# Optimization experiments

Measured on AMD Instinct MI355X. Metric: run time of the kernel, lower is better.

The kernel has to match this reference:

```python
import jax, jax.numpy as jnp
import numpy as np

B, H, D, MAX_N = 2048, 1024, 512, 64
MID_DEC, MID_SP, MID_CD = 768, 512, 512  # build_mlp midmult=1.0 -> mid=(in+out)/2


def setup_inputs() -> dict:
    key = jax.random.key(0)
    ks = jax.random.split(key, 8)
    s = 0.02
    return {
        "z": jax.random.normal(ks[0], (B, H), jnp.float32),
        "key_table": jax.random.normal(ks[1], (MAX_N, H), jnp.float32),
        "sp_w1": jax.random.normal(ks[2], (H, MID_SP), jnp.float32) * s,
        "sp_b1": jnp.zeros((MID_SP,), jnp.float32),
        "sp_g": jnp.ones((MID_SP,), jnp.float32),
        "sp_beta": jnp.zeros((MID_SP,), jnp.float32),
        "sp_w2": jax.random.normal(ks[3], (MID_SP, 1), jnp.float32) * s,
        "sp_b2": jnp.ones((1,), jnp.float32) * 32.0,  # bias so predicted n is mid-range
        "cd_w1": jax.random.normal(ks[4], (1, MID_CD), jnp.float32) * s,
        "cd_b1": jnp.zeros((MID_CD,), jnp.float32),
        "cd_w2": jax.random.normal(ks[5], (MID_CD, H), jnp.float32) * s,
        "cd_b2": jnp.zeros((H,), jnp.float32),
        "dec_w1": jax.random.normal(ks[6], (H, MID_DEC), jnp.float32) * s,
        "dec_b1": jnp.zeros((MID_DEC,), jnp.float32),
        "dec_w2": jax.random.normal(ks[7], (MID_DEC, D), jnp.float32) * s,
        "dec_b2": jnp.zeros((D,), jnp.float32),
    }


def mish(x):
    return x * jnp.tanh(jax.nn.softplus(x))


def layernorm(x, g, b, eps=1e-5):
    mu = x.mean(-1, keepdims=True)
    var = x.var(-1, keepdims=True)
    return (x - mu) * jax.lax.rsqrt(var + eps) * g + b


def reference(z, key_table, sp_w1, sp_b1, sp_g, sp_beta, sp_w2, sp_b2,
              cd_w1, cd_b1, cd_w2, cd_b2, dec_w1, dec_b1, dec_w2, dec_b2):
    # size_pred MLP: Linear -> LayerNorm -> Mish -> Linear
    h = mish(layernorm(z @ sp_w1 + sp_b1, sp_g, sp_beta))
    n_logits = h @ sp_w2 + sp_b2                                  # [B, 1]
    n = jnp.clip(jnp.round(n_logits[:, 0]).astype(jnp.int32), 0, MAX_N)
    n = jax.lax.stop_gradient(n)                                  # int in torch -> no grad
    # shared.cardinality(n): scalar count -> hidden encoding
    nf = n[:, None].astype(z.dtype)
    n_enc = mish(nf @ cd_w1 + cd_b1) @ cd_w2 + cd_b2              # [B, H]
    zc = z - n_enc
    # ragged repeat_interleave + get_key, padded to MAX_N with a validity mask
    kidx = jnp.arange(MAX_N)                                      # positions 0..MAX_N-1
    mask = kidx[None, :] < n[:, None]                             # [B, MAX_N]
    zp = zc[:, None, :] * key_table[None, :, :]                   # [B, MAX_N, H]
    # decoder MLP: Linear -> Mish -> Linear
    x = mish(zp @ dec_w1 + dec_b1) @ dec_w2 + dec_b2              # [B, MAX_N, D]
    x = jnp.where(mask[..., None], x, 0.0).reshape(B * MAX_N, D)
    batch = jnp.where(mask, jnp.arange(B)[:, None], -1).reshape(B * MAX_N)
    return x, batch
```

## Files before the change

kernel.cpp:

```cpp
#include <hip/hip_runtime.h>
#include <stdint.h>

typedef unsigned short ushort_t;
typedef unsigned int uint_t;

#define H_SZ   1024
#define D_OUT  512
#define MAXN   64
#define MIDSP  512
#define MIDCD  512
#define MIDDEC 768

typedef __bf16 bf16x8 __attribute__((ext_vector_type(8)));
typedef float  f32x4  __attribute__((ext_vector_type(4)));

static __device__ __forceinline__ float asf(uint_t u) { union { uint_t i; float f; } c; c.i = u; return c.f; }
static __device__ __forceinline__ uint_t rnbf(float f) {
  union { uint_t i; float f; } c; c.f = f;
  return (c.i + 0x7fffu + ((c.i >> 16) & 1u)) >> 16;
}
static __device__ __forceinline__ ushort_t f2bf(float f) { return (ushort_t)rnbf(f); }
static __device__ __forceinline__ float bf2f(float f) { return asf(rnbf(f) << 16); }
static __device__ __forceinline__ uint_t mul2bf(uint_t a, uint_t b) {
  float a0 = asf(a << 16), a1 = asf(a & 0xffff0000u);
  float b0 = asf(b << 16), b1 = asf(b & 0xffff0000u);
  return rnbf(a0 * b0) | (rnbf(a1 * b1) << 16);
}
static __device__ __forceinline__ double mish_d(double x) { return x * tanh(log1p(exp(x))); }
static __device__ __forceinline__ float mish_f(float x) {
  float t = __expf(x);
  float u = t * t + 2.f * t;
  float r = u / (u + 2.f);
  return (x > 30.f) ? x : x * r;
}

__global__ __launch_bounds__(256) void k_pack1(const float* __restrict__ w1,
                                               ushort_t* __restrict__ pk1) {
  const int t8 = blockIdx.x * 256 + threadIdx.x;
  const int lane = t8 & 63;
  const int ks = (t8 >> 6) & 31;
  const int wp = t8 >> 11;
  const int w = wp / 6, p = wp % 6;
  const int q = lane >> 4, l15 = lane & 15;
  const int row = p * 128 + w * 16 + l15;
  const int colb = ks * 32 + q * 8;
  ushort_t v[8];
#pragma unroll
  for (int e = 0; e < 8; ++e) v[e] = f2bf(w1[(size_t)(colb + e) * 768 + row]);
  *(uint4*)(pk1 + (size_t)t8 * 8) = *(const uint4*)v;
}

__global__ __launch_bounds__(256) void k_pack2(const float* __restrict__ w2,
                                               ushort_t* __restrict__ pk2) {
  const int t8 = blockIdx.x * 256 + threadIdx.x;
  const int lane = t8 & 63;
  const int ki = (t8 >> 6) & 15;
  const int wp = t8 >> 10;
  const int w = wp / 6, p = wp % 6;
  const int ksl = ki >> 2, i = ki & 3;
  const int q = lane >> 4, l15 = lane & 15;
  const int row = w * 64 + i * 16 + l15;
  const int colb = p * 128 + ksl * 32 + q * 8;
  ushort_t v[8];
#pragma unroll
  for (int e = 0; e < 8; ++e) v[e] = f2bf(w2[(size_t)(colb + e) * 512 + row]);
  *(uint4*)(pk2 + (size_t)t8 * 8) = *(const uint4*)v;
}

__global__ __launch_bounds__(256) void k_cvtkey(const float* __restrict__ src, ushort_t* __restrict__ dst) {
  const int i = blockIdx.x * 1024 + threadIdx.x;
#pragma unroll
  for (int j = 0; j < 4; ++j) dst[i + j * 256] = f2bf(src[i + j * 256]);
}

__global__ __launch_bounds__(256) void k_enc(const float* __restrict__ w1, const float* __restrict__ b1,
                                             const float* __restrict__ w2, const float* __restrict__ b2,
                                             float* __restrict__ enc) {
  const int v = blockIdx.x, t = threadIdx.x;
  const int c = blockIdx.y * 256 + t;
  __shared__ float m[MIDCD];
  for (int i = t; i < MIDCD; i += 256) {
    double a = (double)v * (double)w1[i] + (double)b1[i];
    m[i] = (float)mish_d(a);
  }
  __syncthreads();
  double s = (double)b2[c];
  for (int k = 0; k < MIDCD; ++k) s += (double)m[k] * (double)w2[(size_t)k * H_SZ + c];
  enc[(size_t)v * H_SZ + c] = (float)s;
}

__global__ __launch_bounds__(256) void k_npath(
    const float* __restrict__ z, const float* __restrict__ w1, const float* __restrict__ b1,
    const float* __restrict__ g, const float* __restrict__ be,
    const float* __restrict__ w2, const float* __restrict__ b2,
    const float* __restrict__ enc, int* __restrict__ nbuf,
    ushort_t* __restrict__ zc, float* __restrict__ outb) {
  const int t = threadIdx.x;
  const int r0 = blockIdx.x * 4;
  const int lane = t & 63, wv = t >> 6;
  __shared__ float zs[4][H_SZ];
  __shared__ double wred[4];
  __shared__ int n4[4];

#pragma unroll
  for (int i = 0; i < 16; ++i) {
    const int idx = i * 256 + t;
    zs[idx >> 10][idx & 1023] = z[(size_t)r0 * H_SZ + idx];
  }
  __syncthreads();

  const int c0 = t, c1 = t + 256;
  float a0[4], a1[4];
#pragma unroll
  for (int r = 0; r < 4; ++r) { a0[r] = 0.f; a1[r] = 0.f; }

  for (int k = 0; k < H_SZ; k += 4) {
    float4 zr[4];
#pragma unroll
    for (int r = 0; r < 4; ++r) zr[r] = *(const float4*)&zs[r][k];
#pragma unroll
    for (int kk = 0; kk < 4; ++kk) {
      const float w0 = w1[(size_t)(k + kk) * MIDSP + c0];
      const float w1v = w1[(size_t)(k + kk) * MIDSP + c1];
#pragma unroll
      for (int r = 0; r < 4; ++r) {
        const float zk = ((const float*)&zr[r])[kk];
        a0[r] += zk * w0;
        a1[r] += zk * w1v;
      }
    }
  }

  auto block_sum = [&](double v) -> double {
#pragma unroll
    for (int off = 32; off > 0; off >>= 1) v += __shfl_down(v, off, 64);
    if (lane == 0) wred[wv] = v;
    __syncthreads();
    const double s = wred[0] + wred[1] + wred[2] + wred[3];
    __syncthreads();
    return s;
  };

  const double bia0 = (double)b1[c0], bia1 = (double)b1[c1];
  const double g0 = (double)g[c0], g1 = (double)g[c1];
  const double be0 = (double)be[c0], be1 = (double)be[c1];
  const double wv0 = (double)w2[c0], wv1 = (double)w2[c1];
  const double b2v = (double)b2[0];

  for (int r = 0; r < 4; ++r) {
    const double x0 = (double)a0[r] + bia0;
    const double x1 = (double)a1[r] + bia1;
    const double mu = block_sum(x0 + x1) * (1.0 / 512.0);
    const double varr = block_sum((x0 - mu) * (x0 - mu) + (x1 - mu) * (x1 - mu)) * (1.0 / 512.0);
    const double rs = 1.0 / sqrt(varr + 1e-5);
    const double h0 = mish_d((x0 - mu) * rs * g0 + be0);
    const double h1 = mish_d((x1 - mu) * rs * g1 + be1);
    const double logit = block_sum(h0 * wv0 + h1 * wv1) + b2v;
    if (t == 0) n4[r] = (int)fmin(64.0, fmax(0.0, rint(logit)));
  }
  __syncthreads();

  if (t < 4) nbuf[r0 + t] = n4[t];
  {
    const int r = t >> 6, j = t & 63;
    outb[(size_t)(r0 + r) * MAXN + j] = (j < n4[r]) ? (float)(r0 + r) : -1.0f;
  }
#pragma unroll
  for (int i = 0; i < 16; ++i) {
    const int idx = i * 256 + t;
    const int r = idx >> 10, c = idx & 1023;
    zc[(size_t)(r0 + r) * H_SZ + c] = f2bf(zs[r][c] - enc[(size_t)n4[r] * H_SZ + c]);
  }
}

static __device__ __forceinline__ void dec_sweep2(
    char* sA, char* sT,
    const ushort_t* __restrict__ pk1, const float* __restrict__ db1,
    const ushort_t* __restrict__ pk2, const float* __restrict__ db2,
    float* __restrict__ ob, const int tid, const int lim) {
  const int lane = tid & 63;
  const int w = tid >> 6;
  const int q = lane >> 4;
  const int l15 = lane & 15;
  const int x7 = l15 & 7;

  f32x4 z4 = {0.f, 0.f, 0.f, 0.f};
  f32x4 acc2[2][4];
#pragma unroll
  for (int mt = 0; mt < 2; ++mt)
#pragma unroll
    for (int i = 0; i < 4; ++i) acc2[mt][i] = z4;

  for (int p = 0; p < 6; ++p) {
    f32x4 acc0 = z4, acc1 = z4;
    const ushort_t* bp1 = pk1 + ((size_t)(w * 6 + p) << 14) + lane * 8;
    const char* sa0 = sA + (size_t)l15 * 2048;

#pragma unroll 4
    for (int ks = 0; ks < 32; ++ks) {
      bf16x8 bfr = *(const bf16x8*)(bp1 + ks * 512);
      bf16x8 a0 = *(const bf16x8*)(sa0 + (((ks * 4 + q) ^ x7) * 16));
      bf16x8 a1 = *(const bf16x8*)(sa0 + 16 * 2048 + (((ks * 4 + q) ^ x7) * 16));
      acc0 = __builtin_amdgcn_mfma_f32_16x16x32_bf16(a0, bfr, acc0, 0, 0, 0);
      acc1 = __builtin_amdgcn_mfma_f32_16x16x32_bf16(a1, bfr, acc1, 0, 0, 0);
    }

    {
      const int pl = w * 16 + l15;
      const float bias = db1[p * 128 + pl];
      const int c = pl >> 3;
      const int off = (pl & 7) * 2;
#pragma unroll
      for (int r = 0; r < 4; ++r) {
        const int j0 = q * 4 + r;
        *(ushort_t*)(sT + j0 * 256 + ((c ^ (j0 & 7)) * 16 + off)) = f2bf(mish_f(acc0[r] + bias));
        const int j1 = 16 + q * 4 + r;
        *(ushort_t*)(sT + j1 * 256 + ((c ^ (j1 & 7)) * 16 + off)) = f2bf(mish_f(acc1[r] + bias));
      }
    }
    __syncthreads();

    const ushort_t* bp2 = pk2 + ((size_t)(w * 6 + p) << 13) + lane * 8;
    const char* st0 = sT + (size_t)l15 * 256;
#pragma unroll
    for (int ksl = 0; ksl < 4; ++ksl) {
      bf16x8 bfr[4];
#pragma unroll
      for (int i = 0; i < 4; ++i) bfr[i] = *(const bf16x8*)(bp2 + (ksl * 4 + i) * 512);
      bf16x8 a0 = *(const bf16x8*)(st0 + (((ksl * 4 + q) ^ x7) * 16));
      bf16x8 a1 = *(const bf16x8*)(st0 + 16 * 256 + (((ksl * 4 + q) ^ x7) * 16));
#pragma unroll
      for (int i = 0; i < 4; ++i) {
        acc2[0][i] = __builtin_amdgcn_mfma_f32_16x16x32_bf16(a0, bfr[i], acc2[0][i], 0, 0, 0);
        acc2[1][i] = __builtin_amdgcn_mfma_f32_16x16x32_bf16(a1, bfr[i], acc2[1][i], 0, 0, 0);
      }
    }
    __syncthreads();
  }

#pragma unroll
  for (int mt = 0; mt < 2; ++mt)
#pragma unroll
    for (int i = 0; i < 4; ++i) {
      const int col = (w * 4 + i) * 16 + l15;
      const float bias = db2[col];
#pragma unroll
      for (int r = 0; r < 4; ++r) {
        const int j = mt * 16 + q * 4 + r;
        const float v = (j < lim) ? bf2f(acc2[mt][i][r] + bias) : 0.f;
        ob[(size_t)j * D_OUT + col] = v;
      }
    }
}

__global__ __launch_bounds__(512, 4) void k_dec(
    const ushort_t* __restrict__ key, const ushort_t* __restrict__ pk1,
    const float* __restrict__ db1, const ushort_t* __restrict__ pk2,
    const float* __restrict__ db2, const ushort_t* __restrict__ zc,
    const int* __restrict__ nbuf, float* __restrict__ out) {
  __shared__ char sA[65536];
  __shared__ char sT[8192];

  const int tid = threadIdx.x;
  const int b = blockIdx.x;

  int n = nbuf[b];
  n = n < 0 ? 0 : (n > MAXN ? MAXN : n);
  float* ob = out + (size_t)b * (MAXN * D_OUT);

  if (n == 0) {
    const float4 z4f = make_float4(0.f, 0.f, 0.f, 0.f);
#pragma unroll
    for (int i = 0; i < 16; ++i) *(float4*)(ob + i * 2048 + tid * 4) = z4f;
    return;
  }

  const int gj = tid >> 4;
  const int gk = tid & 15;
  const ushort_t* zrow = zc + (size_t)b * H_SZ + gk * 8;
  char* awbase = sA + gj * 2048;
  const int xj = gj & 7;

  {
    const ushort_t* keyrow = key + (size_t)gj * H_SZ + gk * 8;
#pragma unroll
    for (int i = 0; i < 8; ++i) {
      const int c = i * 16 + gk;
      uint4 kv = *(const uint4*)(keyrow + i * 128);
      uint4 zv = *(const uint4*)(zrow + i * 128);
      uint4 r;
      r.x = mul2bf(kv.x, zv.x); r.y = mul2bf(kv.y, zv.y);
      r.z = mul2bf(kv.z, zv.z); r.w = mul2bf(kv.w, zv.w);
      *(uint4*)(awbase + ((c ^ xj) * 16)) = r;
    }
  }
  __syncthreads();
  {
    const int lim = n > 32 ? 32 : n;
    dec_sweep2(sA, sT, pk1, db1, pk2, db2, ob, tid, lim);
  }

  if (n > 32) {
    __syncthreads();
    const ushort_t* keyrow = key + (size_t)(32 + gj) * H_SZ + gk * 8;
#pragma unroll
    for (int i = 0; i < 8; ++i) {
      const int c = i * 16 + gk;
      uint4 kv = *(const uint4*)(keyrow + i * 128);
      uint4 zv = *(const uint4*)(zrow + i * 128);
      uint4 r;
      r.x = mul2bf(kv.x, zv.x); r.y = mul2bf(kv.y, zv.y);
      r.z = mul2bf(kv.z, zv.z); r.w = mul2bf(kv.w, zv.w);
      *(uint4*)(awbase + ((c ^ xj) * 16)) = r;
    }
    __syncthreads();
    dec_sweep2(sA, sT, pk1, db1, pk2, db2, ob + (size_t)32 * D_OUT, tid, n - 32);
  } else {
    float* oz = ob + 32 * D_OUT;
    const float4 z4f = make_float4(0.f, 0.f, 0.f, 0.f);
#pragma unroll
    for (int i = 0; i < 8; ++i) *(float4*)(oz + i * 2048 + tid * 4) = z4f;
  }
}

extern "C" void kernel_launch(void* const* d_in, const int* in_sizes, int n_in,
                              void* d_out, int out_size, void* d_ws, size_t ws_size,
                              hipStream_t stream) {
  const float* z      = (const float*)d_in[0];
  const float* key    = (const float*)d_in[1];
  const float* sp_w1  = (const float*)d_in[2];
  const float* sp_b1  = (const float*)d_in[3];
  const float* sp_g   = (const float*)d_in[4];
  const float* sp_be  = (const float*)d_in[5];
  const float* sp_w2  = (const float*)d_in[6];
  const float* sp_b2  = (const float*)d_in[7];
  const float* cd_w1  = (const float*)d_in[8];
  const float* cd_b1  = (const float*)d_in[9];
  const float* cd_w2  = (const float*)d_in[10];
  const float* cd_b2  = (const float*)d_in[11];
  const float* dec_w1 = (const float*)d_in[12];
  const float* dec_b1 = (const float*)d_in[13];
  const float* dec_w2 = (const float*)d_in[14];
  const float* dec_b2 = (const float*)d_in[15];

  char* ws = (char*)d_ws;
  float*    enc   = (float*)(ws + 0);
  int*      nbuf  = (int*)(ws + 266240);
  ushort_t* zc    = (ushort_t*)(ws + 274432);
  ushort_t* pk1   = (ushort_t*)(ws + 4468736);
  ushort_t* pk2   = (ushort_t*)(ws + 6041600);
  ushort_t* keyb  = (ushort_t*)(ws + 6828032);

  float* out  = (float*)d_out;
  float* outb = out + (size_t)2048 * MAXN * D_OUT;

  (void)in_sizes; (void)n_in; (void)out_size; (void)ws_size;

  k_pack1<<<384, 256, 0, stream>>>(dec_w1, pk1);
  k_pack2<<<192, 256, 0, stream>>>(dec_w2, pk2);
  k_cvtkey<<<64, 256, 0, stream>>>(key, keyb);
  k_enc<<<dim3(65, 4), 256, 0, stream>>>(cd_w1, cd_b1, cd_w2, cd_b2, enc);
  k_npath<<<512, 256, 0, stream>>>(z, sp_w1, sp_b1, sp_g, sp_be, sp_w2, sp_b2, enc, nbuf, zc, outb);
  k_dec<<<2048, 512, 0, stream>>>(keyb, pk1, dec_b1, pk2, dec_b2, zc, nbuf, out);
}
```

Measured before the change: 731.6 us.

## Decode two batch rows per block to reuse weight fragments; fuse prep kernels

The decoder kernel now handles two batch rows per workgroup, so each loaded weight fragment from both decoder layers feeds four MFMAs instead of two. This halves the weight traffic from L2/global per unit of work. In exchange, LDS use per block roughly doubles (about 144 KB), which allows fewer resident blocks per CU. The second 32-row phase also runs whenever either row of the pair needs it, and the n==0 early exit is gone. Separately, the three weight and key conversion kernels are merged into one launch to save launch overhead.

After: 778.5 us. 1.06x slower.

```diff
diff --git a/kernel.cpp b/kernel.cpp
--- a/kernel.cpp
+++ b/kernel.cpp
@@ -34,43 +34,42 @@
   return (x > 30.f) ? x : x * r;
 }
 
-__global__ __launch_bounds__(256) void k_pack1(const float* __restrict__ w1,
-                                               ushort_t* __restrict__ pk1) {
-  const int t8 = blockIdx.x * 256 + threadIdx.x;
-  const int lane = t8 & 63;
-  const int ks = (t8 >> 6) & 31;
-  const int wp = t8 >> 11;
-  const int w = wp / 6, p = wp % 6;
-  const int q = lane >> 4, l15 = lane & 15;
-  const int row = p * 128 + w * 16 + l15;
-  const int colb = ks * 32 + q * 8;
-  ushort_t v[8];
-#pragma unroll
-  for (int e = 0; e < 8; ++e) v[e] = f2bf(w1[(size_t)(colb + e) * 768 + row]);
-  *(uint4*)(pk1 + (size_t)t8 * 8) = *(const uint4*)v;
-}
-
-__global__ __launch_bounds__(256) void k_pack2(const float* __restrict__ w2,
-                                               ushort_t* __restrict__ pk2) {
-  const int t8 = blockIdx.x * 256 + threadIdx.x;
-  const int lane = t8 & 63;
-  const int ki = (t8 >> 6) & 15;
-  const int wp = t8 >> 10;
-  const int w = wp / 6, p = wp % 6;
-  const int ksl = ki >> 2, i = ki & 3;
-  const int q = lane >> 4, l15 = lane & 15;
-  const int row = w * 64 + i * 16 + l15;
-  const int colb = p * 128 + ksl * 32 + q * 8;
-  ushort_t v[8];
-#pragma unroll
-  for (int e = 0; e < 8; ++e) v[e] = f2bf(w2[(size_t)(colb + e) * 512 + row]);
-  *(uint4*)(pk2 + (size_t)t8 * 8) = *(const uint4*)v;
-}
-
-__global__ __launch_bounds__(256) void k_cvtkey(const float* __restrict__ src, ushort_t* __restrict__ dst) {
-  const int i = blockIdx.x * 1024 + threadIdx.x;
-#pragma unroll
-  for (int j = 0; j < 4; ++j) dst[i + j * 256] = f2bf(src[i + j * 256]);
+__global__ __launch_bounds__(256) void k_prep(const float* __restrict__ w1, ushort_t* __restrict__ pk1,
+                                              const float* __restrict__ w2, ushort_t* __restrict__ pk2,
+                                              const float* __restrict__ keysrc, ushort_t* __restrict__ keyb) {
+  const int bid = blockIdx.x;
+  if (bid < 384) {
+    const int t8 = bid * 256 + threadIdx.x;
+    const int lane = t8 & 63;
+    const int ks = (t8 >> 6) & 31;
+    const int wp = t8 >> 11;
+    const int w = wp / 6, p = wp % 6;
+    const int q = lane >> 4, l15 = lane & 15;
+    const int row = p * 128 + w * 16 + l15;
+    const int colb = ks * 32 + q * 8;
+    ushort_t v[8];
+#pragma unroll
+    for (int e = 0; e < 8; ++e) v[e] = f2bf(w1[(size_t)(colb + e) * 768 + row]);
+    *(uint4*)(pk1 + (size_t)t8 * 8) = *(const uint4*)v;
+  } else if (bid < 576) {
+    const int t8 = (bid - 384) * 256 + threadIdx.x;
+    const int lane = t8 & 63;
+    const int ki = (t8 >> 6) & 15;
+    const int wp = t8 >> 10;
+    const int w = wp / 6, p = wp % 6;
+    const int ksl = ki >> 2, i = ki & 3;
+    const int q = lane >> 4, l15 = lane & 15;
+    const int row = w * 64 + i * 16 + l15;
+    const int colb = p * 128 + ksl * 32 + q * 8;
+    ushort_t v[8];
+#pragma unroll
+    for (int e = 0; e < 8; ++e) v[e] = f2bf(w2[(size_t)(colb + e) * 512 + row]);
+    *(uint4*)(pk2 + (size_t)t8 * 8) = *(const uint4*)v;
+  } else {
+    const int i = (bid - 576) * 1024 + threadIdx.x;
+#pragma unroll
+    for (int j = 0; j < 4; ++j) keyb[i + j * 256] = f2bf(keysrc[i + j * 256]);
+  }
 }
 
 __global__ __launch_bounds__(256) void k_enc(const float* __restrict__ w1, const float* __restrict__ b1,
@@ -173,11 +172,12 @@
   }
 }
 
-static __device__ __forceinline__ void dec_sweep2(
+static __device__ __forceinline__ void dec_pair(
     char* sA, char* sT,
     const ushort_t* __restrict__ pk1, const float* __restrict__ db1,
     const ushort_t* __restrict__ pk2, const float* __restrict__ db2,
-    float* __restrict__ ob, const int tid, const int lim) {
+    float* __restrict__ ob0, float* __restrict__ ob1,
+    const int tid, const int lim0, const int lim1) {
   const int lane = tid & 63;
   const int w = tid >> 6;
   const int q = lane >> 4;
@@ -185,24 +185,37 @@
   const int x7 = l15 & 7;
 
   f32x4 z4 = {0.f, 0.f, 0.f, 0.f};
-  f32x4 acc2[2][4];
-#pragma unroll
-  for (int mt = 0; mt < 2; ++mt)
-#pragma unroll
-    for (int i = 0; i < 4; ++i) acc2[mt][i] = z4;
+  f32x4 acc2[2][2][4];
+#pragma unroll
+  for (int bb = 0; bb < 2; ++bb)
+#pragma unroll
+    for (int mt = 0; mt < 2; ++mt)
+#pragma unroll
+      for (int i = 0; i < 4; ++i) acc2[bb][mt][i] = z4;
 
   for (int p = 0; p < 6; ++p) {
-    f32x4 acc0 = z4, acc1 = z4;
+    f32x4 acc[2][2];
+#pragma unroll
+    for (int bb = 0; bb < 2; ++bb)
+#pragma unroll
+      for (int mt = 0; mt < 2; ++mt) acc[bb][mt] = z4;
+
     const ushort_t* bp1 = pk1 + ((size_t)(w * 6 + p) << 14) + lane * 8;
-    const char* sa0 = sA + (size_t)l15 * 2048;
+    const char* saA = sA + (size_t)l15 * 2048;
+    const char* saB = sA + 65536 + (size_t)l15 * 2048;
 
 #pragma unroll 4
     for (int ks = 0; ks < 32; ++ks) {
       bf16x8 bfr = *(const bf16x8*)(bp1 + ks * 512);
-      bf16x8 a0 = *(const bf16x8*)(sa0 + (((ks * 4 + q) ^ x7) * 16));
-      bf16x8 a1 = *(const bf16x8*)(sa0 + 16 * 2048 + (((ks * 4 + q) ^ x7) * 16));
-      acc0 = __builtin_amdgcn_mfma_f32_16x16x32_bf16(a0, bfr, acc0, 0, 0, 0);
-      acc1 = __builtin_amdgcn_mfma_f32_16x16x32_bf16(a1, bfr, acc1, 0, 0, 0);
+      const int co = ((ks * 4 + q) ^ x7) * 16;
+      bf16x8 a00 = *(const bf16x8*)(saA + co);
+      bf16x8 a01 = *(const bf16x8*)(saA + 16 * 2048 + co);
+      bf16x8 a10 = *(const bf16x8*)(saB + co);
+      bf16x8 a11 = *(const bf16x8*)(saB + 16 * 2048 + co);
+      acc[0][0] = __builtin_amdgcn_mfma_f32_16x16x32_bf16(a00, bfr, acc[0][0], 0, 0, 0);
+      acc[0][1] = __builtin_amdgcn_mfma_f32_16x16x32_bf16(a01, bfr, acc[0][1], 0, 0, 0);
+      acc[1][0] = __builtin_amdgcn_mfma_f32_16x16x32_bf16(a10, bfr, acc[1][0], 0, 0, 0);
+      acc[1][1] = __builtin_amdgcn_mfma_f32_16x16x32_bf16(a11, bfr, acc[1][1], 0, 0, 0);
     }
 
     {
@@ -211,115 +224,119 @@
       const int c = pl >> 3;
       const int off = (pl & 7) * 2;
 #pragma unroll
-      for (int r = 0; r < 4; ++r) {
-        const int j0 = q * 4 + r;
-        *(ushort_t*)(sT + j0 * 256 + ((c ^ (j0 & 7)) * 16 + off)) = f2bf(mish_f(acc0[r] + bias));
-        const int j1 = 16 + q * 4 + r;
-        *(ushort_t*)(sT + j1 * 256 + ((c ^ (j1 & 7)) * 16 + off)) = f2bf(mish_f(acc1[r] + bias));
-      }
+      for (int bb = 0; bb < 2; ++bb)
+#pragma unroll
+        for (int mt = 0; mt < 2; ++mt)
+#pragma unroll
+          for (int r = 0; r < 4; ++r) {
+            const int j = mt * 16 + q * 4 + r;
+            *(ushort_t*)(sT + bb * 8192 + j * 256 + ((c ^ (j & 7)) * 16 + off)) =
+                f2bf(mish_f(acc[bb][mt][r] + bias));
+          }
     }
     __syncthreads();
 
     const ushort_t* bp2 = pk2 + ((size_t)(w * 6 + p) << 13) + lane * 8;
-    const char* st0 = sT + (size_t)l15 * 256;
 #pragma unroll
     for (int ksl = 0; ksl < 4; ++ksl) {
       bf16x8 bfr[4];
 #pragma unroll
       for (int i = 0; i < 4; ++i) bfr[i] = *(const bf16x8*)(bp2 + (ksl * 4 + i) * 512);
-      bf16x8 a0 = *(const bf16x8*)(st0 + (((ksl * 4 + q) ^ x7) * 16));
-      bf16x8 a1 = *(const bf16x8*)(st0 + 16 * 256 + (((ksl * 4 + q) ^ x7) * 16));
+      const int co = ((ksl * 4 + q) ^ x7) * 16;
+      bf16x8 a00 = *(const bf16x8*)(sT + (size_t)l15 * 256 + co);
+      bf16x8 a01 = *(const bf16x8*)(sT + (size_t)(16 + l15) * 256 + co);
+      bf16x8 a10 = *(const bf16x8*)(sT + 8192 + (size_t)l15 * 256 + co);
+      bf16x8 a11 = *(const bf16x8*)(sT + 8192 + (size_t)(16 + l15) * 256 + co);
 #pragma unroll
       for (int i = 0; i < 4; ++i) {
-        acc2[0][i] = __builtin_amdgcn_mfma_f32_16x16x32_bf16(a0, bfr[i], acc2[0][i], 0, 0, 0);
-        acc2[1][i] = __builtin_amdgcn_mfma_f32_16x16x32_bf16(a1, bfr[i], acc2[1][i], 0, 0, 0);
+        acc2[0][0][i] = __builtin_amdgcn_mfma_f32_16x16x32_bf16(a00, bfr[i], acc2[0][0][i], 0, 0, 0);
+        acc2[0][1][i] = __builtin_amdgcn_mfma_f32_16x16x32_bf16(a01, bfr[i], acc2[0][1][i], 0, 0, 0);
+        acc2[1][0][i] = __builtin_amdgcn_mfma_f32_16x16x32_bf16(a10, bfr[i], acc2[1][0][i], 0, 0, 0);
+        acc2[1][1][i] = __builtin_amdgcn_mfma_f32_16x16x32_bf16(a11, bfr[i], acc2[1][1][i], 0, 0, 0);
       }
     }
     __syncthreads();
   }
 
 #pragma unroll
-  for (int mt = 0; mt < 2; ++mt)
-#pragma unroll
-    for (int i = 0; i < 4; ++i) {
-      const int col = (w * 4 + i) * 16 + l15;
-      const float bias = db2[col];
-#pragma unroll
-      for (int r = 0; r < 4; ++r) {
-        const int j = mt * 16 + q * 4 + r;
-        const float v = (j < lim) ? bf2f(acc2[mt][i][r] + bias) : 0.f;
-        ob[(size_t)j * D_OUT + col] = v;
+  for (int bb = 0; bb < 2; ++bb) {
+    float* ob = bb ? ob1 : ob0;
+    const int lim = bb ? lim1 : lim0;
+#pragma unroll
+    for (int mt = 0; mt < 2; ++mt)
+#pragma unroll
+      for (int i = 0; i < 4; ++i) {
+        const int col = (w * 4 + i) * 16 + l15;
+        const float bias = db2[col];
+#pragma unroll
+        for (int r = 0; r < 4; ++r) {
+          const int j = mt * 16 + q * 4 + r;
+          const float v = (j < lim) ? bf2f(acc2[bb][mt][i][r] + bias) : 0.f;
+          ob[(size_t)j * D_OUT + col] = v;
+        }
       }
-    }
-}
-
-__global__ __launch_bounds__(512, 4) void k_dec(
+  }
+}
+
+__global__ __launch_bounds__(512, 2) void k_dec(
     const ushort_t* __restrict__ key, const ushort_t* __restrict__ pk1,
     const float* __restrict__ db1, const ushort_t* __restrict__ pk2,
     const float* __restrict__ db2, const ushort_t* __restrict__ zc,
     const int* __restrict__ nbuf, float* __restrict__ out) {
-  __shared__ char sA[65536];
-  __shared__ char sT[8192];
+  __shared__ char sA[131072];
+  __shared__ char sT[16384];
 
   const int tid = threadIdx.x;
-  const int b = blockIdx.x;
-
-  int n = nbuf[b];
-  n = n < 0 ? 0 : (n > MAXN ? MAXN : n);
-  float* ob = out + (size_t)b * (MAXN * D_OUT);
-
-  if (n == 0) {
-    const float4 z4f = make_float4(0.f, 0.f, 0.f, 0.f);
-#pragma unroll
-    for (int i = 0; i < 16; ++i) *(float4*)(ob + i * 2048 + tid * 4) = z4f;
-    return;
-  }
-
-  const int gj = tid >> 4;
-  const int gk = tid & 15;
-  const ushort_t* zrow = zc + (size_t)b * H_SZ + gk * 8;
+  const int b0 = blockIdx.x * 2, b1 = b0 + 1;
+
+  int n0 = nbuf[b0]; n0 = n0 < 0 ? 0 : (n0 > MAXN ? MAXN : n0);
+  int n1 = nbuf[b1]; n1 = n1 < 0 ? 0 : (n1 > MAXN ? MAXN : n1);
+  float* ob0 = out + (size_t)b0 * (MAXN * D_OUT);
+  float* ob1 = out + (size_t)b1 * (MAXN * D_OUT);
+
+  const int gj = tid >> 3;
+  const int gk = tid & 7;
+  const int brow = gj & 31;
+  const ushort_t* zrow = zc + (size_t)(gj < 32 ? b0 : b1) * H_SZ + gk * 8;
   char* awbase = sA + gj * 2048;
   const int xj = gj & 7;
 
-  {
-    const ushort_t* keyrow = key + (size_t)gj * H_SZ + gk * 8;
-#pragma unroll
-    for (int i = 0; i < 8; ++i) {
-      const int c = i * 16 + gk;
-      uint4 kv = *(const uint4*)(keyrow + i * 128);
-      uint4 zv = *(const uint4*)(zrow + i * 128);
+  auto agen = [&](int ph) {
+    const ushort_t* keyrow = key + (size_t)(ph * 32 + brow) * H_SZ + gk * 8;
+#pragma unroll
+    for (int i = 0; i < 16; ++i) {
+      const int c = i * 8 + gk;
+      uint4 kv = *(const uint4*)(keyrow + i * 64);
+      uint4 zv = *(const uint4*)(zrow + i * 64);
       uint4 r;
       r.x = mul2bf(kv.x, zv.x); r.y = mul2bf(kv.y, zv.y);
       r.z = mul2bf(kv.z, zv.z); r.w = mul2bf(kv.w, zv.w);
       *(uint4*)(awbase + ((c ^ xj) * 16)) = r;
     }
-  }
+  };
+
+  agen(0);
   __syncthreads();
   {
-    const int lim = n > 32 ? 32 : n;
-    dec_sweep2(sA, sT, pk1, db1, pk2, db2, ob, tid, lim);
-  }
-
-  if (n > 32) {
-    __syncthreads();
-    const ushort_t* keyrow = key + (size_t)(32 + gj) * H_SZ + gk * 8;
+    const int l0 = n0 > 32 ? 32 : n0;
+    const int l1 = n1 > 32 ? 32 : n1;
+    dec_pair(sA, sT, pk1, db1, pk2, db2, ob0, ob1, tid, l0, l1);
+  }
+
+  if (n0 > 32 || n1 > 32) {
+    agen(1);
+    __syncthreads();
+    const int l0 = n0 > 32 ? n0 - 32 : 0;
+    const int l1 = n1 > 32 ? n1 - 32 : 0;
+    dec_pair(sA, sT, pk1, db1, pk2, db2,
+             ob0 + (size_t)32 * D_OUT, ob1 + (size_t)32 * D_OUT, tid, l0, l1);
+  } else {
+    const float4 z4f = make_float4(0.f, 0.f, 0.f, 0.f);
 #pragma unroll
     for (int i = 0; i < 8; ++i) {
-      const int c = i * 16 + gk;
-      uint4 kv = *(const uint4*)(keyrow + i * 128);
-      uint4 zv = *(const uint4*)(zrow + i * 128);
-      uint4 r;
-      r.x = mul2bf(kv.x, zv.x); r.y = mul2bf(kv.y, zv.y);
-      r.z = mul2bf(kv.z, zv.z); r.w = mul2bf(kv.w, zv.w);
-      *(uint4*)(awbase + ((c ^ xj) * 16)) = r;
-    }
-    __syncthreads();
-    dec_sweep2(sA, sT, pk1, db1, pk2, db2, ob + (size_t)32 * D_OUT, tid, n - 32);
-  } else {
-    float* oz = ob + 32 * D_OUT;
-    const float4 z4f = make_float4(0.f, 0.f, 0.f, 0.f);
-#pragma unroll
-    for (int i = 0; i < 8; ++i) *(float4*)(oz + i * 2048 + tid * 4) = z4f;
+      *(float4*)(ob0 + 32 * D_OUT + i * 2048 + tid * 4) = z4f;
+      *(float4*)(ob1 + 32 * D_OUT + i * 2048 + tid * 4) = z4f;
+    }
   }
 }
 
@@ -356,10 +373,8 @@
 
   (void)in_sizes; (void)n_in; (void)out_size; (void)ws_size;
 
-  k_pack1<<<384, 256, 0, stream>>>(dec_w1, pk1);
-  k_pack2<<<192, 256, 0, stream>>>(dec_w2, pk2);
-  k_cvtkey<<<64, 256, 0, stream>>>(key, keyb);
+  k_prep<<<640, 256, 0, stream>>>(dec_w1, pk1, dec_w2, pk2, key, keyb);
   k_enc<<<dim3(65, 4), 256, 0, stream>>>(cd_w1, cd_b1, cd_w2, cd_b2, enc);
   k_npath<<<512, 256, 0, stream>>>(z, sp_w1, sp_b1, sp_g, sp_be, sp_w2, sp_b2, enc, nbuf, zc, outb);
-  k_dec<<<2048, 512, 0, stream>>>(keyb, pk1, dec_b1, pk2, dec_b2, zc, nbuf, out);
-}
+  k_dec<<<1024, 512, 0, stream>>>(keyb, pk1, dec_b1, pk2, dec_b2, zc, nbuf, out);
+}
```

## Merge weight-prep kernels and compute three decoder N-panels per A-fragment load

Applied to the files above, without the earlier changes.

The three small prep kernels (w1 pack, w2 pack, key conversion) are merged into one launch selected by block index, removing two launch gaps. In the decoder sweep, the first GEMM now processes three 128-column panels at once, so each A fragment read from LDS feeds six MFMAs instead of two. The second GEMM still runs per panel. This cuts LDS reads and loop overhead in the first GEMM but adds accumulator and B-fragment registers under launch_bounds(512,4), which may cause spills or lower occupancy.

After: 789.0 us. 1.08x slower.

```diff
diff --git a/kernel.cpp b/kernel.cpp
--- a/kernel.cpp
+++ b/kernel.cpp
@@ -34,43 +34,42 @@
   return (x > 30.f) ? x : x * r;
 }
 
-__global__ __launch_bounds__(256) void k_pack1(const float* __restrict__ w1,
-                                               ushort_t* __restrict__ pk1) {
-  const int t8 = blockIdx.x * 256 + threadIdx.x;
-  const int lane = t8 & 63;
-  const int ks = (t8 >> 6) & 31;
-  const int wp = t8 >> 11;
-  const int w = wp / 6, p = wp % 6;
-  const int q = lane >> 4, l15 = lane & 15;
-  const int row = p * 128 + w * 16 + l15;
-  const int colb = ks * 32 + q * 8;
-  ushort_t v[8];
-#pragma unroll
-  for (int e = 0; e < 8; ++e) v[e] = f2bf(w1[(size_t)(colb + e) * 768 + row]);
-  *(uint4*)(pk1 + (size_t)t8 * 8) = *(const uint4*)v;
-}
-
-__global__ __launch_bounds__(256) void k_pack2(const float* __restrict__ w2,
-                                               ushort_t* __restrict__ pk2) {
-  const int t8 = blockIdx.x * 256 + threadIdx.x;
-  const int lane = t8 & 63;
-  const int ki = (t8 >> 6) & 15;
-  const int wp = t8 >> 10;
-  const int w = wp / 6, p = wp % 6;
-  const int ksl = ki >> 2, i = ki & 3;
-  const int q = lane >> 4, l15 = lane & 15;
-  const int row = w * 64 + i * 16 + l15;
-  const int colb = p * 128 + ksl * 32 + q * 8;
-  ushort_t v[8];
-#pragma unroll
-  for (int e = 0; e < 8; ++e) v[e] = f2bf(w2[(size_t)(colb + e) * 512 + row]);
-  *(uint4*)(pk2 + (size_t)t8 * 8) = *(const uint4*)v;
-}
-
-__global__ __launch_bounds__(256) void k_cvtkey(const float* __restrict__ src, ushort_t* __restrict__ dst) {
-  const int i = blockIdx.x * 1024 + threadIdx.x;
-#pragma unroll
-  for (int j = 0; j < 4; ++j) dst[i + j * 256] = f2bf(src[i + j * 256]);
+__global__ __launch_bounds__(256) void k_prep(const float* __restrict__ w1, ushort_t* __restrict__ pk1,
+                                              const float* __restrict__ w2, ushort_t* __restrict__ pk2,
+                                              const float* __restrict__ keysrc, ushort_t* __restrict__ keyb) {
+  const int bid = blockIdx.x;
+  if (bid < 384) {
+    const int t8 = bid * 256 + threadIdx.x;
+    const int lane = t8 & 63;
+    const int ks = (t8 >> 6) & 31;
+    const int wp = t8 >> 11;
+    const int w = wp / 6, p = wp % 6;
+    const int q = lane >> 4, l15 = lane & 15;
+    const int row = p * 128 + w * 16 + l15;
+    const int colb = ks * 32 + q * 8;
+    ushort_t v[8];
+#pragma unroll
+    for (int e = 0; e < 8; ++e) v[e] = f2bf(w1[(size_t)(colb + e) * 768 + row]);
+    *(uint4*)(pk1 + (size_t)t8 * 8) = *(const uint4*)v;
+  } else if (bid < 576) {
+    const int t8 = (bid - 384) * 256 + threadIdx.x;
+    const int lane = t8 & 63;
+    const int ki = (t8 >> 6) & 15;
+    const int wp = t8 >> 10;
+    const int w = wp / 6, p = wp % 6;
+    const int ksl = ki >> 2, i = ki & 3;
+    const int q = lane >> 4, l15 = lane & 15;
+    const int row = w * 64 + i * 16 + l15;
+    const int colb = p * 128 + ksl * 32 + q * 8;
+    ushort_t v[8];
+#pragma unroll
+    for (int e = 0; e < 8; ++e) v[e] = f2bf(w2[(size_t)(colb + e) * 512 + row]);
+    *(uint4*)(pk2 + (size_t)t8 * 8) = *(const uint4*)v;
+  } else {
+    const int i = (bid - 576) * 1024 + threadIdx.x;
+#pragma unroll
+    for (int j = 0; j < 4; ++j) keyb[i + j * 256] = f2bf(keysrc[i + j * 256]);
+  }
 }
 
 __global__ __launch_bounds__(256) void k_enc(const float* __restrict__ w1, const float* __restrict__ b1,
@@ -191,51 +190,70 @@
 #pragma unroll
     for (int i = 0; i < 4; ++i) acc2[mt][i] = z4;
 
-  for (int p = 0; p < 6; ++p) {
-    f32x4 acc0 = z4, acc1 = z4;
-    const ushort_t* bp1 = pk1 + ((size_t)(w * 6 + p) << 14) + lane * 8;
+  for (int g = 0; g < 2; ++g) {
+    f32x4 acc[3][2];
+#pragma unroll
+    for (int j = 0; j < 3; ++j)
+#pragma unroll
+      for (int mt = 0; mt < 2; ++mt) acc[j][mt] = z4;
+
+    const ushort_t* bpa = pk1 + ((size_t)(w * 6 + g * 3 + 0) << 14) + lane * 8;
+    const ushort_t* bpb = pk1 + ((size_t)(w * 6 + g * 3 + 1) << 14) + lane * 8;
+    const ushort_t* bpc = pk1 + ((size_t)(w * 6 + g * 3 + 2) << 14) + lane * 8;
     const char* sa0 = sA + (size_t)l15 * 2048;
 
 #pragma unroll 4
     for (int ks = 0; ks < 32; ++ks) {
-      bf16x8 bfr = *(const bf16x8*)(bp1 + ks * 512);
-      bf16x8 a0 = *(const bf16x8*)(sa0 + (((ks * 4 + q) ^ x7) * 16));
-      bf16x8 a1 = *(const bf16x8*)(sa0 + 16 * 2048 + (((ks * 4 + q) ^ x7) * 16));
-      acc0 = __builtin_amdgcn_mfma_f32_16x16x32_bf16(a0, bfr, acc0, 0, 0, 0);
-      acc1 = __builtin_amdgcn_mfma_f32_16x16x32_bf16(a1, bfr, acc1, 0, 0, 0);
-    }
-
-    {
-      const int pl = w * 16 + l15;
-      const float bias = db1[p * 128 + pl];
-      const int c = pl >> 3;
-      const int off = (pl & 7) * 2;
-#pragma unroll
-      for (int r = 0; r < 4; ++r) {
-        const int j0 = q * 4 + r;
-        *(ushort_t*)(sT + j0 * 256 + ((c ^ (j0 & 7)) * 16 + off)) = f2bf(mish_f(acc0[r] + bias));
-        const int j1 = 16 + q * 4 + r;
-        *(ushort_t*)(sT + j1 * 256 + ((c ^ (j1 & 7)) * 16 + off)) = f2bf(mish_f(acc1[r] + bias));
+      const int co = ((ks * 4 + q) ^ x7) * 16;
+      bf16x8 a0 = *(const bf16x8*)(sa0 + co);
+      bf16x8 a1 = *(const bf16x8*)(sa0 + 16 * 2048 + co);
+      bf16x8 b0 = *(const bf16x8*)(bpa + ks * 512);
+      bf16x8 b1 = *(const bf16x8*)(bpb + ks * 512);
+      bf16x8 b2 = *(const bf16x8*)(bpc + ks * 512);
+      acc[0][0] = __builtin_amdgcn_mfma_f32_16x16x32_bf16(a0, b0, acc[0][0], 0, 0, 0);
+      acc[0][1] = __builtin_amdgcn_mfma_f32_16x16x32_bf16(a1, b0, acc[0][1], 0, 0, 0);
+      acc[1][0] = __builtin_amdgcn_mfma_f32_16x16x32_bf16(a0, b1, acc[1][0], 0, 0, 0);
+      acc[1][1] = __builtin_amdgcn_mfma_f32_16x16x32_bf16(a1, b1, acc[1][1], 0, 0, 0);
+      acc[2][0] = __builtin_amdgcn_mfma_f32_16x16x32_bf16(a0, b2, acc[2][0], 0, 0, 0);
+      acc[2][1] = __builtin_amdgcn_mfma_f32_16x16x32_bf16(a1, b2, acc[2][1], 0, 0, 0);
+    }
+
+#pragma unroll
+    for (int j = 0; j < 3; ++j) {
+      const int p = g * 3 + j;
+      {
+        const int pl = w * 16 + l15;
+        const float bias = db1[p * 128 + pl];
+        const int c = pl >> 3;
+        const int off = (pl & 7) * 2;
+#pragma unroll
+        for (int r = 0; r < 4; ++r) {
+          const int j0 = q * 4 + r;
+          *(ushort_t*)(sT + j0 * 256 + ((c ^ (j0 & 7)) * 16 + off)) = f2bf(mish_f(acc[j][0][r] + bias));
+          const int j1 = 16 + q * 4 + r;
+          *(ushort_t*)(sT + j1 * 256 + ((c ^ (j1 & 7)) * 16 + off)) = f2bf(mish_f(acc[j][1][r] + bias));
+        }
       }
-    }
-    __syncthreads();
-
-    const ushort_t* bp2 = pk2 + ((size_t)(w * 6 + p) << 13) + lane * 8;
-    const char* st0 = sT + (size_t)l15 * 256;
-#pragma unroll
-    for (int ksl = 0; ksl < 4; ++ksl) {
-      bf16x8 bfr[4];
-#pragma unroll
-      for (int i = 0; i < 4; ++i) bfr[i] = *(const bf16x8*)(bp2 + (ksl * 4 + i) * 512);
-      bf16x8 a0 = *(const bf16x8*)(st0 + (((ksl * 4 + q) ^ x7) * 16));
-      bf16x8 a1 = *(const bf16x8*)(st0 + 16 * 256 + (((ksl * 4 + q) ^ x7) * 16));
-#pragma unroll
-      for (int i = 0; i < 4; ++i) {
-        acc2[0][i] = __builtin_amdgcn_mfma_f32_16x16x32_bf16(a0, bfr[i], acc2[0][i], 0, 0, 0);
-        acc2[1][i] = __builtin_amdgcn_mfma_f32_16x16x32_bf16(a1, bfr[i], acc2[1][i], 0, 0, 0);
+      __syncthreads();
+
+      const ushort_t* bp2 = pk2 + ((size_t)(w * 6 + p) << 13) + lane * 8;
+      const char* st0 = sT + (size_t)l15 * 256;
+#pragma unroll
+      for (int ksl = 0; ksl < 4; ++ksl) {
+        bf16x8 bfr[4];
+#pragma unroll
+        for (int i = 0; i < 4; ++i) bfr[i] = *(const bf16x8*)(bp2 + (ksl * 4 + i) * 512);
+        const int co = ((ksl * 4 + q) ^ x7) * 16;
+        bf16x8 ta0 = *(const bf16x8*)(st0 + co);
+        bf16x8 ta1 = *(const bf16x8*)(st0 + 16 * 256 + co);
+#pragma unroll
+        for (int i = 0; i < 4; ++i) {
+          acc2[0][i] = __builtin_amdgcn_mfma_f32_16x16x32_bf16(ta0, bfr[i], acc2[0][i], 0, 0, 0);
+          acc2[1][i] = __builtin_amdgcn_mfma_f32_16x16x32_bf16(ta1, bfr[i], acc2[1][i], 0, 0, 0);
+        }
       }
-    }
-    __syncthreads();
+      __syncthreads();
+    }
   }
 
 #pragma unroll
@@ -356,9 +374,7 @@
 
   (void)in_sizes; (void)n_in; (void)out_size; (void)ws_size;
 
-  k_pack1<<<384, 256, 0, stream>>>(dec_w1, pk1);
-  k_pack2<<<192, 256, 0, stream>>>(dec_w2, pk2);
-  k_cvtkey<<<64, 256, 0, stream>>>(key, keyb);
+  k_prep<<<640, 256, 0, stream>>>(dec_w1, pk1, dec_w2, pk2, key, keyb);
   k_enc<<<dim3(65, 4), 256, 0, stream>>>(cd_w1, cd_b1, cd_w2, cd_b2, enc);
   k_npath<<<512, 256, 0, stream>>>(z, sp_w1, sp_b1, sp_g, sp_be, sp_w2, sp_b2, enc, nbuf, zc, outb);
   k_dec<<<2048, 512, 0, stream>>>(keyb, pk1, dec_b1, pk2, dec_b2, zc, nbuf, out);
```
